# Kernel optimization log

Measured on AMD Instinct MI355X. Metric: run time of the kernel, lower is better.

## Reference

```python
import jax, jax.numpy as jnp
import numpy as np

P = 7                 # ROI pool output size (7,7)
SCALE = 1.0 / 16.0    # spatial_scale


def setup_inputs() -> dict:
    key = jax.random.key(0)
    ks = jax.random.split(key, 8)
    C, H, W = 512, 32, 32
    N = 128
    n_classes = 21
    features = jax.random.normal(ks[0], (1, C, H, W), dtype=jnp.float32)
    img_h, img_w = H * 16, W * 16  # image-space size implied by stride 16
    u = jax.random.uniform(ks[1], (N, 4), dtype=jnp.float32)
    x1 = u[:, 0] * (img_w - 32.0)
    y1 = u[:, 1] * (img_h - 32.0)
    x2 = x1 + 16.0 + u[:, 2] * (img_w - 1.0 - 16.0 - x1)
    y2 = y1 + 16.0 + u[:, 3] * (img_h - 1.0 - 16.0 - y1)
    rois = jnp.stack([jnp.zeros(N), x1, y1, x2, y2], axis=1).astype(jnp.float32)
    d_in = C * P * P

    def lin(k, fi, fo):
        return (jax.random.normal(k, (fi, fo), dtype=jnp.float32) / np.float32(np.sqrt(fi)))

    return {
        "features": features,
        "rois": rois,
        "W6": lin(ks[2], d_in, 4096), "b6": jnp.zeros((4096,), jnp.float32),
        "W7": lin(ks[3], 4096, 4096), "b7": jnp.zeros((4096,), jnp.float32),
        "Ws": lin(ks[4], 4096, n_classes), "bs": jnp.zeros((n_classes,), jnp.float32),
        "Wb": lin(ks[5], 4096, n_classes * 4), "bb": jnp.zeros((n_classes * 4,), jnp.float32),
    }


def roi_adaptive_max_pool(features, rois):
    # features: [1, C, H, W]; rois: [N, 5] (col 0 = batch idx, stripped as in torch)
    feats = features[0]                       # [C, H, W]
    C, H, W = feats.shape
    boxes = jnp.floor(rois[:, 1:] * SCALE).astype(jnp.int32)  # .long() trunc, coords >= 0
    x1, y1, x2, y2 = boxes[:, 0], boxes[:, 1], boxes[:, 2], boxes[:, 3]
    h = y2 - y1 + 1  # inclusive slicing roi[1]:roi[3]+1
    w = x2 - x1 + 1
    i = jnp.arange(P)
    # AdaptiveMaxPool2d bin boundaries: start = floor(i*h/P), end = ceil((i+1)*h/P)
    rs = y1[:, None] + (i[None, :] * h[:, None]) // P                       # [N, P]
    re = y1[:, None] + ((i[None, :] + 1) * h[:, None] + (P - 1)) // P
    cs = x1[:, None] + (i[None, :] * w[:, None]) // P
    ce = x1[:, None] + ((i[None, :] + 1) * w[:, None] + (P - 1)) // P
    MBr = -(-H // P)  # max rows per bin
    MBc = -(-W // P)  # max cols per bin
    neg_inf = jnp.float32(-jnp.inf)
    # row stage: max over each bin's rows, all columns kept
    ridx = rs[:, :, None] + jnp.arange(MBr)                                 # [N, P, MBr]
    rmask = ridx < re[:, :, None]
    ridx = jnp.clip(ridx, 0, H - 1)
    rowg = feats[:, ridx, :]                                                # [C, N, P, MBr, W]
    rowg = jnp.where(rmask[None, :, :, :, None], rowg, neg_inf)
    rowmax = rowg.max(axis=3).transpose(1, 0, 2, 3)                         # [N, C, P, W]
    # col stage: max over each bin's columns
    cidx = cs[:, :, None] + jnp.arange(MBc)                                 # [N, P, MBc]
    cmask = cidx < ce[:, :, None]
    cidx = jnp.clip(cidx, 0, W - 1)
    colg = jax.vmap(lambda rm, ci: rm[:, :, ci])(rowmax, cidx)              # [N, C, P, P, MBc]
    colg = jnp.where(cmask[:, None, None, :, :], colg, neg_inf)
    return colg.max(axis=-1)                                                # [N, C, P, P]


def reference(features, rois, W6, b6, W7, b7, Ws, bs, Wb, bb):
    pooled = roi_adaptive_max_pool(features, rois)          # [N, C, 7, 7]
    x = pooled.reshape(pooled.shape[0], -1)                 # [N, C*49]
    x = jax.nn.relu(x @ W6 + b6)                            # fc6 (dropout off: eval)
    x = jax.nn.relu(x @ W7 + b7)                            # fc7
    cls_prob = jax.nn.softmax(x @ Ws + bs, axis=1)          # [N, n_classes]
    bbox_pred = x @ Wb + bb                                 # [N, n_classes*4]
    return jnp.concatenate([cls_prob, bbox_pred], axis=1)   # [N, n_classes*5]
```

## Files before the change

kernel.cpp:

```cpp
#include <hip/hip_runtime.h>
#include <stdint.h>
#include <math.h>


typedef short short8 __attribute__((ext_vector_type(8)));
typedef float f32x4 __attribute__((ext_vector_type(4)));

__device__ __forceinline__ uint32_t pack_hilo(float x) {
  uint32_t xb = __float_as_uint(x);
  uint32_t hi = (xb + 0x7fffu + ((xb >> 16) & 1u)) >> 16;
  float hf = __uint_as_float(hi << 16);
  float d = x - hf;
  uint32_t db = __float_as_uint(d);
  uint32_t lo = (db + 0x7fffu + ((db >> 16) & 1u)) >> 16;
  return (lo << 16) | (hi & 0xffffu);
}

__device__ __forceinline__ void pack_pair(float x0, float x1,
                                          uint32_t& hw, uint32_t& lw) {
  uint32_t u0 = __float_as_uint(x0), u1 = __float_as_uint(x1);
  uint32_t r0 = (u0 + 0x7fffu + ((u0 >> 16) & 1u)) & 0xffff0000u;
  uint32_t r1 = (u1 + 0x7fffu + ((u1 >> 16) & 1u)) & 0xffff0000u;
  hw = r1 | (r0 >> 16);
  float d0 = x0 - __uint_as_float(r0);
  float d1 = x1 - __uint_as_float(r1);
  uint32_t v0 = __float_as_uint(d0), v1 = __float_as_uint(d1);
  uint32_t s0 = (v0 + 0x7fffu + ((v0 >> 16) & 1u)) & 0xffff0000u;
  uint32_t s1 = (v1 + 0x7fffu + ((v1 >> 16) & 1u)) & 0xffff0000u;
  lw = s1 | (s0 >> 16);
}

__device__ __forceinline__ short8 lds_frag(const uint32_t* p) {
  union { uint4 q; short8 s; } x;
  x.q = *(const uint4*)p;
  return x.s;
}

__global__ void transpose_k(const float* __restrict__ in, float* __restrict__ out) {
  __shared__ float sm[64][65];
  int bc = blockIdx.x & 7;
  int bp = blockIdx.x >> 3;
  int c0 = bc * 64, p0 = bp * 64;
  int tx = threadIdx.x & 63, ty = threadIdx.x >> 6;
  for (int r = ty; r < 64; r += 4)
    sm[r][tx] = in[(size_t)(c0 + r) * 1024 + p0 + tx];
  __syncthreads();
  for (int r = ty; r < 64; r += 4)
    out[(size_t)(p0 + r) * 512 + c0 + tx] = sm[tx][r];
}

__global__ void pool_k(const float* __restrict__ feats_t, const float* __restrict__ rois,
                       uint32_t* __restrict__ Ahi, uint32_t* __restrict__ Alo) {
  int n = blockIdx.x >> 1, half = blockIdx.x & 1;
  int t = threadIdx.x;
  int c = half * 256 + t;
  __shared__ uint32_t sm[256 * 49];

  float r1 = rois[n * 5 + 1], r2 = rois[n * 5 + 2];
  float r3 = rois[n * 5 + 3], r4 = rois[n * 5 + 4];
  int x1 = (int)floorf(r1 * 0.0625f);
  int y1 = (int)floorf(r2 * 0.0625f);
  int x2 = (int)floorf(r3 * 0.0625f);
  int y2 = (int)floorf(r4 * 0.0625f);
  int h = y2 - y1 + 1, w = x2 - x1 + 1;

  for (int cell = 0; cell < 49; ++cell) {
    int i = cell / 7, j = cell % 7;
    int rs = y1 + (i * h) / 7;
    int re = y1 + ((i + 1) * h + 6) / 7;  re = min(re, rs + 5);
    int cs = x1 + (j * w) / 7;
    int ce = x1 + ((j + 1) * w + 6) / 7;  ce = min(ce, cs + 5);
    float m = -INFINITY;
    for (int r = rs; r < re; ++r)
      for (int cc = cs; cc < ce; ++cc)
        m = fmaxf(m, feats_t[(size_t)(r * 32 + cc) * 512 + c]);
    sm[t * 49 + cell] = pack_hilo(m);
  }
  __syncthreads();
  uint32_t* dh = Ahi + (size_t)n * 12544 + (size_t)half * 6272;
  uint32_t* dl = Alo + (size_t)n * 12544 + (size_t)half * 6272;
  for (int i = t; i < 6272; i += 256) {
    uint32_t w0 = sm[2 * i], w1 = sm[2 * i + 1];
    dh[i] = __builtin_amdgcn_perm(w1, w0, 0x05040100u);
    dl[i] = __builtin_amdgcn_perm(w1, w0, 0x07060302u);
  }
}

__global__ __launch_bounds__(256, 2)
void gemm_splitk(const uint32_t* __restrict__ Ahi, const uint32_t* __restrict__ Alo,
                 const float* __restrict__ W, float* __restrict__ partials,
                 int Khalf, int ksteps, int ksh) {
  const int t = threadIdx.x;
  const int wvid = t >> 6, lane = t & 63;
  const int nb = blockIdx.x >> ksh;
  const int ks = blockIdx.x & ((1 << ksh) - 1);
  const int n0 = nb << 7;
  const int kbase2 = ks * (ksteps << 4);

  __shared__ uint32_t lds[4][128 * 20];

  const int nloc = t & 127, khalf = t >> 7;
  const float* wg = W + ((size_t)kbase2 * 2 + khalf * 16) * 4096 + n0 + nloc;

  const int arow = wvid * 32 + (lane >> 1);
  const int aco = (lane & 1) * 8;
  const uint32_t* agh = Ahi + (size_t)arow * Khalf + kbase2 + aco;
  const uint32_t* agl = Alo + (size_t)arow * Khalf + kbase2 + aco;

  f32x4 acc[2][8];
#pragma unroll
  for (int i = 0; i < 2; i++)
#pragma unroll
    for (int j = 0; j < 8; j++) acc[i][j] = f32x4{0.f, 0.f, 0.f, 0.f};

  float wcA[16], wcB[16];
  uint4 aA[4], aB[4];

  auto issue = [&](float (&wc)[16], uint4 (&av)[4], int s) {
    const float* wp = wg + (size_t)s * 32 * 4096;
#pragma unroll
    for (int i = 0; i < 16; i++) wc[i] = __builtin_nontemporal_load(wp + (size_t)i * 4096);
    const uint32_t* ph = agh + (size_t)s * 16;
    const uint32_t* pl = agl + (size_t)s * 16;
    av[0] = *(const uint4*)(ph);
    av[1] = *(const uint4*)(ph + 4);
    av[2] = *(const uint4*)(pl);
    av[3] = *(const uint4*)(pl + 4);
  };

  auto pack_w = [&](float (&wc)[16], uint32_t (&hw)[8], uint32_t (&lw)[8]) {
#pragma unroll
    for (int j = 0; j < 8; j++) pack_pair(wc[2 * j], wc[2 * j + 1], hw[j], lw[j]);
  };
  auto store_tile = [&](uint32_t (&hw)[8], uint32_t (&lw)[8], uint4 (&av)[4]) {
    *(uint4*)&lds[2][nloc * 20 + khalf * 8]     = make_uint4(hw[0], hw[1], hw[2], hw[3]);
    *(uint4*)&lds[2][nloc * 20 + khalf * 8 + 4] = make_uint4(hw[4], hw[5], hw[6], hw[7]);
    *(uint4*)&lds[3][nloc * 20 + khalf * 8]     = make_uint4(lw[0], lw[1], lw[2], lw[3]);
    *(uint4*)&lds[3][nloc * 20 + khalf * 8 + 4] = make_uint4(lw[4], lw[5], lw[6], lw[7]);
    *(uint4*)&lds[0][arow * 20 + aco]     = av[0];
    *(uint4*)&lds[0][arow * 20 + aco + 4] = av[1];
    *(uint4*)&lds[1][arow * 20 + aco]     = av[2];
    *(uint4*)&lds[1][arow * 20 + aco + 4] = av[3];
  };

  const int lr = lane & 15, kk = lane >> 4;

  auto mfma_tile = [&]() {
    short8 ahif[2], alof[2];
#pragma unroll
    for (int fm = 0; fm < 2; fm++) {
      int rb = (wvid * 32 + fm * 16 + lr) * 20 + kk * 4;
      ahif[fm] = lds_frag(&lds[0][rb]);
      alof[fm] = lds_frag(&lds[1][rb]);
    }
#pragma unroll
    for (int fn = 0; fn < 8; fn++) {
      int rb = (fn * 16 + lr) * 20 + kk * 4;
      short8 bhi = lds_frag(&lds[2][rb]);
      short8 blo = lds_frag(&lds[3][rb]);
#pragma unroll
      for (int fm = 0; fm < 2; fm++) {
        acc[fm][fn] = __builtin_amdgcn_mfma_f32_16x16x32_bf16(ahif[fm], bhi, acc[fm][fn], 0, 0, 0);
        acc[fm][fn] = __builtin_amdgcn_mfma_f32_16x16x32_bf16(ahif[fm], blo, acc[fm][fn], 0, 0, 0);
        acc[fm][fn] = __builtin_amdgcn_mfma_f32_16x16x32_bf16(alof[fm], bhi, acc[fm][fn], 0, 0, 0);
      }
    }
  };

  issue(wcA, aA, 0);
  if (ksteps > 1) issue(wcB, aB, 1);
  {
    uint32_t hw[8], lw[8];
    pack_w(wcA, hw, lw);
    store_tile(hw, lw, aA);
  }
  __syncthreads();

  for (int s = 0; s < ksteps; s += 2) {
    if (s + 2 < ksteps) issue(wcA, aA, s + 2);
    mfma_tile();
    if (s + 1 < ksteps) {
      uint32_t hw[8], lw[8];
      pack_w(wcB, hw, lw);
      __syncthreads();
      store_tile(hw, lw, aB);
      __syncthreads();
      if (s + 3 < ksteps) issue(wcB, aB, s + 3);
      mfma_tile();
      if (s + 2 < ksteps) {
        uint32_t hw2[8], lw2[8];
        pack_w(wcA, hw2, lw2);
        __syncthreads();
        store_tile(hw2, lw2, aA);
        __syncthreads();
      }
    }
  }

  float* pout = partials + (size_t)ks * 524288;
  const int rq = lane >> 4;
#pragma unroll
  for (int fm = 0; fm < 2; fm++)
#pragma unroll
    for (int fn = 0; fn < 8; fn++)
#pragma unroll
      for (int r = 0; r < 4; r++) {
        int row = wvid * 32 + fm * 16 + rq * 4 + r;
        int col = n0 + fn * 16 + lr;
        __builtin_nontemporal_store(acc[fm][fn][r], pout + (size_t)row * 4096 + col);
      }
}

__global__ void reduce_k(const float* __restrict__ partials, const float* __restrict__ bias,
                         uint32_t* __restrict__ outhi, uint32_t* __restrict__ outlo,
                         float* __restrict__ fout, int KS) {
  int idx = blockIdx.x * 256 + threadIdx.x;
  int base = idx * 4;
  float4 s = make_float4(0.f, 0.f, 0.f, 0.f);
  for (int k = 0; k < KS; k++) {
    const float4 p = *(const float4*)(partials + (size_t)k * 524288 + base);
    s.x += p.x; s.y += p.y; s.z += p.z; s.w += p.w;
  }
  const float4 bv = *(const float4*)(bias + (base & 4095));
  s.x = fmaxf(s.x + bv.x, 0.f); s.y = fmaxf(s.y + bv.y, 0.f);
  s.z = fmaxf(s.z + bv.z, 0.f); s.w = fmaxf(s.w + bv.w, 0.f);
  if (outhi) {
    uint32_t h0, l0, h1, l1;
    pack_pair(s.x, s.y, h0, l0);
    pack_pair(s.z, s.w, h1, l1);
    *(uint2*)(outhi + idx * 2) = make_uint2(h0, h1);
    *(uint2*)(outlo + idx * 2) = make_uint2(l0, l1);
  } else {
    *(float4*)(fout + base) = s;
  }
}

__global__ void heads_k(const float* __restrict__ x2, const float* __restrict__ Ws,
                        const float* __restrict__ bs, const float* __restrict__ Wb,
                        const float* __restrict__ bb, float* __restrict__ out) {
  int n = blockIdx.x, t = threadIdx.x;
  int j = t & 127, kq = t >> 7;
  float a0 = 0.f, a1 = 0.f, a2 = 0.f, a3 = 0.f;
  if (j < 105) {
    const float* xp = x2 + (size_t)n * 4096 + kq * 1024;
    const float* wq;
    int stride;
    if (j < 21) { wq = Ws + (size_t)kq * 1024 * 21 + j; stride = 21; }
    else        { wq = Wb + (size_t)kq * 1024 * 84 + (j - 21); stride = 84; }
    for (int k = 0; k < 1024; k += 4) {
      const float4 xv = *(const float4*)(xp + k);
      a0 += xv.x * wq[(size_t)k * stride];
      a1 += xv.y * wq[(size_t)(k + 1) * stride];
      a2 += xv.z * wq[(size_t)(k + 2) * stride];
      a3 += xv.w * wq[(size_t)(k + 3) * stride];
    }
  }
  __shared__ float sacc[512];
  __shared__ float slog[105];
  sacc[t] = (a0 + a1) + (a2 + a3);
  __syncthreads();
  if (t < 105)
    slog[t] = (sacc[t] + sacc[t + 128]) + (sacc[t + 256] + sacc[t + 384]) +
              (t < 21 ? bs[t] : bb[t - 21]);
  __syncthreads();
  if (t < 105) {
    float v = slog[t];
    if (t < 21) {
      float m = slog[0];
      for (int q = 1; q < 21; q++) m = fmaxf(m, slog[q]);
      float ssum = 0.f;
      for (int q = 0; q < 21; q++) ssum += expf(slog[q] - m);
      v = expf(v - m) / ssum;
    }
    out[(size_t)n * 105 + t] = v;
  }
}

extern "C" void kernel_launch(void* const* d_in, const int* in_sizes, int n_in,
                              void* d_out, int out_size, void* d_ws, size_t ws_size,
                              hipStream_t stream) {
  const float* feats = (const float*)d_in[0];
  const float* rois  = (const float*)d_in[1];
  const float* W6 = (const float*)d_in[2];
  const float* b6 = (const float*)d_in[3];
  const float* W7 = (const float*)d_in[4];
  const float* b7 = (const float*)d_in[5];
  const float* Wsp = (const float*)d_in[6];
  const float* bsp = (const float*)d_in[7];
  const float* Wbp = (const float*)d_in[8];
  const float* bbp = (const float*)d_in[9];
  float* out = (float*)d_out;

  char* ws = (char*)d_ws;
  size_t o = 0;
  float*    feats_t = (float*)(ws + o);    o += (size_t)512 * 1024 * 4;
  uint32_t* Ahi     = (uint32_t*)(ws + o); o += (size_t)128 * 12544 * 4;
  uint32_t* Alo     = (uint32_t*)(ws + o); o += (size_t)128 * 12544 * 4;
  uint32_t* A2hi    = (uint32_t*)(ws + o); o += (size_t)128 * 2048 * 4;
  uint32_t* A2lo    = (uint32_t*)(ws + o); o += (size_t)128 * 2048 * 4;
  float*    x2      = (float*)(ws + o);    o += (size_t)128 * 4096 * 4;
  size_t fixed = o;
  int KS = 16;
  while (KS > 1 && fixed + (size_t)KS * 524288 * 4 > ws_size) KS >>= 1;
  float* partials = (float*)(ws + o);
  int ksh = (KS == 16) ? 4 : (KS == 8) ? 3 : (KS == 4) ? 2 : (KS == 2) ? 1 : 0;
  int ksh7 = (ksh > 3) ? 3 : ksh;
  int KS7 = 1 << ksh7;

  hipLaunchKernelGGL(transpose_k, dim3(128), dim3(256), 0, stream, feats, feats_t);
  hipLaunchKernelGGL(pool_k, dim3(256), dim3(256), 0, stream, feats_t, rois, Ahi, Alo);
  hipLaunchKernelGGL(gemm_splitk, dim3(32 << ksh), dim3(256), 0, stream,
                     Ahi, Alo, W6, partials, 12544, 25088 / (KS * 32), ksh);
  hipLaunchKernelGGL(reduce_k, dim3(512), dim3(256), 0, stream,
                     partials, b6, A2hi, A2lo, (float*)nullptr, KS);
  hipLaunchKernelGGL(gemm_splitk, dim3(32 << ksh7), dim3(256), 0, stream,
                     A2hi, A2lo, W7, partials, 2048, 4096 / (KS7 * 32), ksh7);
  hipLaunchKernelGGL(reduce_k, dim3(512), dim3(256), 0, stream,
                     partials, b7, (uint32_t*)nullptr, (uint32_t*)nullptr, x2, KS7);
  hipLaunchKernelGGL(heads_k, dim3(128), dim3(512), 0, stream,
                     x2, Wsp, bsp, Wbp, bbp, out);
}
```

Baseline: 932.0 us.

## Drop LDS staging in split-K GEMM; load MFMA fragments straight from registers/global

The GEMM kernel no longer stages A and W tiles through shared memory with barriers. Each wave now loads its W fragment directly into registers in MFMA B-operand order and packs it in place. A is read directly from global memory in a new fragment-friendly transposed layout (k-quad major, row, 4 words), which pool_k and reduce_k now write. fc7 also uses the full split-K factor instead of capping it at 8. The aim is to remove LDS traffic and __syncthreads stalls. The cost is redundant global/L2 reads of A across waves, more registers, and scattered writes in pool and reduce.

Result: faster. 899.7 us (-3.5%).

```diff
diff --git a/kernel.cpp b/kernel.cpp
--- a/kernel.cpp
+++ b/kernel.cpp
@@ -30,9 +30,14 @@
   lw = s1 | (s0 >> 16);
 }
 
-__device__ __forceinline__ short8 lds_frag(const uint32_t* p) {
+__device__ __forceinline__ short8 u4_to_s8(uint4 q) {
   union { uint4 q; short8 s; } x;
-  x.q = *(const uint4*)p;
+  x.q = q;
+  return x.s;
+}
+__device__ __forceinline__ short8 mk8(uint32_t a, uint32_t b, uint32_t c, uint32_t d) {
+  union { uint32_t u[4]; short8 s; } x;
+  x.u[0] = a; x.u[1] = b; x.u[2] = c; x.u[3] = d;
   return x.s;
 }
 
@@ -50,7 +55,7 @@
 }
 
 __global__ void pool_k(const float* __restrict__ feats_t, const float* __restrict__ rois,
-                       uint32_t* __restrict__ Ahi, uint32_t* __restrict__ Alo) {
+                       uint32_t* __restrict__ AhiT, uint32_t* __restrict__ AloT) {
   int n = blockIdx.x >> 1, half = blockIdx.x & 1;
   int t = threadIdx.x;
   int c = half * 256 + t;
@@ -77,135 +82,95 @@
     sm[t * 49 + cell] = pack_hilo(m);
   }
   __syncthreads();
-  uint32_t* dh = Ahi + (size_t)n * 12544 + (size_t)half * 6272;
-  uint32_t* dl = Alo + (size_t)n * 12544 + (size_t)half * 6272;
   for (int i = t; i < 6272; i += 256) {
     uint32_t w0 = sm[2 * i], w1 = sm[2 * i + 1];
-    dh[i] = __builtin_amdgcn_perm(w1, w0, 0x05040100u);
-    dl[i] = __builtin_amdgcn_perm(w1, w0, 0x07060302u);
+    int kp = half * 6272 + i;
+    size_t ad = ((size_t)(kp >> 2) * 128 + n) * 4 + (kp & 3);
+    AhiT[ad] = __builtin_amdgcn_perm(w1, w0, 0x05040100u);
+    AloT[ad] = __builtin_amdgcn_perm(w1, w0, 0x07060302u);
   }
 }
 
 __global__ __launch_bounds__(256, 2)
-void gemm_splitk(const uint32_t* __restrict__ Ahi, const uint32_t* __restrict__ Alo,
-                 const float* __restrict__ W, float* __restrict__ partials,
-                 int Khalf, int ksteps, int ksh) {
-  const int t = threadIdx.x;
-  const int wvid = t >> 6, lane = t & 63;
-  const int nb = blockIdx.x >> ksh;
-  const int ks = blockIdx.x & ((1 << ksh) - 1);
-  const int n0 = nb << 7;
-  const int kbase2 = ks * (ksteps << 4);
-
-  __shared__ uint32_t lds[4][128 * 20];
-
-  const int nloc = t & 127, khalf = t >> 7;
-  const float* wg = W + ((size_t)kbase2 * 2 + khalf * 16) * 4096 + n0 + nloc;
-
-  const int arow = wvid * 32 + (lane >> 1);
-  const int aco = (lane & 1) * 8;
-  const uint32_t* agh = Ahi + (size_t)arow * Khalf + kbase2 + aco;
-  const uint32_t* agl = Alo + (size_t)arow * Khalf + kbase2 + aco;
-
-  f32x4 acc[2][8];
-#pragma unroll
-  for (int i = 0; i < 2; i++)
-#pragma unroll
-    for (int j = 0; j < 8; j++) acc[i][j] = f32x4{0.f, 0.f, 0.f, 0.f};
-
-  float wcA[16], wcB[16];
-  uint4 aA[4], aB[4];
-
-  auto issue = [&](float (&wc)[16], uint4 (&av)[4], int s) {
-    const float* wp = wg + (size_t)s * 32 * 4096;
-#pragma unroll
-    for (int i = 0; i < 16; i++) wc[i] = __builtin_nontemporal_load(wp + (size_t)i * 4096);
-    const uint32_t* ph = agh + (size_t)s * 16;
-    const uint32_t* pl = agl + (size_t)s * 16;
-    av[0] = *(const uint4*)(ph);
-    av[1] = *(const uint4*)(ph + 4);
-    av[2] = *(const uint4*)(pl);
-    av[3] = *(const uint4*)(pl + 4);
+void gemm_nb(const uint32_t* __restrict__ AhiT, const uint32_t* __restrict__ AloT,
+             const float* __restrict__ W, float* __restrict__ partials,
+             int ksteps, int ksh) {
+  const int t = threadIdx.x, wv = t >> 6, lane = t & 63;
+  const int lr = lane & 15, kk = lane >> 4;
+  const int nb = blockIdx.x >> ksh, ks = blockIdx.x & ((1 << ksh) - 1);
+  const int n0 = (nb << 7) + wv * 32;
+  const int kp40 = ks * ksteps * 4;
+
+  const float* wg = W + ((size_t)kp40 * 8 + kk * 8) * 4096 + n0 + lr;
+  const uint32_t* ah = AhiT + ((size_t)(kp40 + kk) * 128 + lr) * 4;
+  const uint32_t* al = AloT + ((size_t)(kp40 + kk) * 128 + lr) * 4;
+
+  f32x4 acc[8][2];
+#pragma unroll
+  for (int i = 0; i < 8; i++)
+#pragma unroll
+    for (int j = 0; j < 2; j++) acc[i][j] = f32x4{0.f, 0.f, 0.f, 0.f};
+
+  float wA[16], wB[16];
+
+  auto wissue = [&](float (&wc)[16], int s) {
+    const float* p = wg + (size_t)s * 32 * 4096;
+#pragma unroll
+    for (int fn = 0; fn < 2; fn++)
+#pragma unroll
+      for (int j = 0; j < 8; j++)
+        wc[fn * 8 + j] = __builtin_nontemporal_load(p + (size_t)j * 4096 + fn * 16);
   };
 
-  auto pack_w = [&](float (&wc)[16], uint32_t (&hw)[8], uint32_t (&lw)[8]) {
-#pragma unroll
-    for (int j = 0; j < 8; j++) pack_pair(wc[2 * j], wc[2 * j + 1], hw[j], lw[j]);
+  auto do_tile = [&](int s, float (&wc)[16]) {
+    uint4 ahv[8], alv[8];
+    const uint32_t* pa = ah + (size_t)s * 2048;
+    const uint32_t* pl = al + (size_t)s * 2048;
+#pragma unroll
+    for (int fm = 0; fm < 8; fm++) {
+      ahv[fm] = *(const uint4*)(pa + fm * 64);
+      alv[fm] = *(const uint4*)(pl + fm * 64);
+    }
+    uint32_t bh[2][4], bl[2][4];
+#pragma unroll
+    for (int fn = 0; fn < 2; fn++)
+#pragma unroll
+      for (int jj = 0; jj < 4; jj++)
+        pack_pair(wc[fn * 8 + 2 * jj], wc[fn * 8 + 2 * jj + 1], bh[fn][jj], bl[fn][jj]);
+#pragma unroll
+    for (int fn = 0; fn < 2; fn++) {
+      short8 b_hi = mk8(bh[fn][0], bh[fn][1], bh[fn][2], bh[fn][3]);
+      short8 b_lo = mk8(bl[fn][0], bl[fn][1], bl[fn][2], bl[fn][3]);
+#pragma unroll
+      for (int fm = 0; fm < 8; fm++) {
+        short8 a_hi = u4_to_s8(ahv[fm]);
+        short8 a_lo = u4_to_s8(alv[fm]);
+        acc[fm][fn] = __builtin_amdgcn_mfma_f32_16x16x32_bf16(a_hi, b_hi, acc[fm][fn], 0, 0, 0);
+        acc[fm][fn] = __builtin_amdgcn_mfma_f32_16x16x32_bf16(a_hi, b_lo, acc[fm][fn], 0, 0, 0);
+        acc[fm][fn] = __builtin_amdgcn_mfma_f32_16x16x32_bf16(a_lo, b_hi, acc[fm][fn], 0, 0, 0);
+      }
+    }
   };
-  auto store_tile = [&](uint32_t (&hw)[8], uint32_t (&lw)[8], uint4 (&av)[4]) {
-    *(uint4*)&lds[2][nloc * 20 + khalf * 8]     = make_uint4(hw[0], hw[1], hw[2], hw[3]);
-    *(uint4*)&lds[2][nloc * 20 + khalf * 8 + 4] = make_uint4(hw[4], hw[5], hw[6], hw[7]);
-    *(uint4*)&lds[3][nloc * 20 + khalf * 8]     = make_uint4(lw[0], lw[1], lw[2], lw[3]);
-    *(uint4*)&lds[3][nloc * 20 + khalf * 8 + 4] = make_uint4(lw[4], lw[5], lw[6], lw[7]);
-    *(uint4*)&lds[0][arow * 20 + aco]     = av[0];
-    *(uint4*)&lds[0][arow * 20 + aco + 4] = av[1];
-    *(uint4*)&lds[1][arow * 20 + aco]     = av[2];
-    *(uint4*)&lds[1][arow * 20 + aco + 4] = av[3];
-  };
-
-  const int lr = lane & 15, kk = lane >> 4;
-
-  auto mfma_tile = [&]() {
-    short8 ahif[2], alof[2];
-#pragma unroll
-    for (int fm = 0; fm < 2; fm++) {
-      int rb = (wvid * 32 + fm * 16 + lr) * 20 + kk * 4;
-      ahif[fm] = lds_frag(&lds[0][rb]);
-      alof[fm] = lds_frag(&lds[1][rb]);
-    }
-#pragma unroll
-    for (int fn = 0; fn < 8; fn++) {
-      int rb = (fn * 16 + lr) * 20 + kk * 4;
-      short8 bhi = lds_frag(&lds[2][rb]);
-      short8 blo = lds_frag(&lds[3][rb]);
-#pragma unroll
-      for (int fm = 0; fm < 2; fm++) {
-        acc[fm][fn] = __builtin_amdgcn_mfma_f32_16x16x32_bf16(ahif[fm], bhi, acc[fm][fn], 0, 0, 0);
-        acc[fm][fn] = __builtin_amdgcn_mfma_f32_16x16x32_bf16(ahif[fm], blo, acc[fm][fn], 0, 0, 0);
-        acc[fm][fn] = __builtin_amdgcn_mfma_f32_16x16x32_bf16(alof[fm], bhi, acc[fm][fn], 0, 0, 0);
-      }
-    }
-  };
-
-  issue(wcA, aA, 0);
-  if (ksteps > 1) issue(wcB, aB, 1);
-  {
-    uint32_t hw[8], lw[8];
-    pack_w(wcA, hw, lw);
-    store_tile(hw, lw, aA);
-  }
-  __syncthreads();
-
+
+  wissue(wA, 0);
   for (int s = 0; s < ksteps; s += 2) {
-    if (s + 2 < ksteps) issue(wcA, aA, s + 2);
-    mfma_tile();
+    if (s + 1 < ksteps) wissue(wB, s + 1);
+    do_tile(s, wA);
     if (s + 1 < ksteps) {
-      uint32_t hw[8], lw[8];
-      pack_w(wcB, hw, lw);
-      __syncthreads();
-      store_tile(hw, lw, aB);
-      __syncthreads();
-      if (s + 3 < ksteps) issue(wcB, aB, s + 3);
-      mfma_tile();
-      if (s + 2 < ksteps) {
-        uint32_t hw2[8], lw2[8];
-        pack_w(wcA, hw2, lw2);
-        __syncthreads();
-        store_tile(hw2, lw2, aA);
-        __syncthreads();
-      }
+      if (s + 2 < ksteps) wissue(wA, s + 2);
+      do_tile(s + 1, wB);
     }
   }
 
   float* pout = partials + (size_t)ks * 524288;
   const int rq = lane >> 4;
 #pragma unroll
-  for (int fm = 0; fm < 2; fm++)
-#pragma unroll
-    for (int fn = 0; fn < 8; fn++)
+  for (int fm = 0; fm < 8; fm++)
+#pragma unroll
+    for (int fn = 0; fn < 2; fn++)
 #pragma unroll
       for (int r = 0; r < 4; r++) {
-        int row = wvid * 32 + fm * 16 + rq * 4 + r;
+        int row = fm * 16 + rq * 4 + r;
         int col = n0 + fn * 16 + lr;
         __builtin_nontemporal_store(acc[fm][fn][r], pout + (size_t)row * 4096 + col);
       }
@@ -228,8 +193,10 @@
     uint32_t h0, l0, h1, l1;
     pack_pair(s.x, s.y, h0, l0);
     pack_pair(s.z, s.w, h1, l1);
-    *(uint2*)(outhi + idx * 2) = make_uint2(h0, h1);
-    *(uint2*)(outlo + idx * 2) = make_uint2(l0, l1);
+    int r = base >> 12, c = base & 4095, kp0 = c >> 1;
+    size_t ad = ((size_t)(kp0 >> 2) * 128 + r) * 4 + (kp0 & 3);
+    *(uint2*)(outhi + ad) = make_uint2(h0, h1);
+    *(uint2*)(outlo + ad) = make_uint2(l0, l1);
   } else {
     *(float4*)(fout + base) = s;
   }
@@ -294,8 +261,8 @@
   char* ws = (char*)d_ws;
   size_t o = 0;
   float*    feats_t = (float*)(ws + o);    o += (size_t)512 * 1024 * 4;
-  uint32_t* Ahi     = (uint32_t*)(ws + o); o += (size_t)128 * 12544 * 4;
-  uint32_t* Alo     = (uint32_t*)(ws + o); o += (size_t)128 * 12544 * 4;
+  uint32_t* AhiT    = (uint32_t*)(ws + o); o += (size_t)128 * 12544 * 4;
+  uint32_t* AloT    = (uint32_t*)(ws + o); o += (size_t)128 * 12544 * 4;
   uint32_t* A2hi    = (uint32_t*)(ws + o); o += (size_t)128 * 2048 * 4;
   uint32_t* A2lo    = (uint32_t*)(ws + o); o += (size_t)128 * 2048 * 4;
   float*    x2      = (float*)(ws + o);    o += (size_t)128 * 4096 * 4;
@@ -304,19 +271,17 @@
   while (KS > 1 && fixed + (size_t)KS * 524288 * 4 > ws_size) KS >>= 1;
   float* partials = (float*)(ws + o);
   int ksh = (KS == 16) ? 4 : (KS == 8) ? 3 : (KS == 4) ? 2 : (KS == 2) ? 1 : 0;
-  int ksh7 = (ksh > 3) ? 3 : ksh;
-  int KS7 = 1 << ksh7;
 
   hipLaunchKernelGGL(transpose_k, dim3(128), dim3(256), 0, stream, feats, feats_t);
-  hipLaunchKernelGGL(pool_k, dim3(256), dim3(256), 0, stream, feats_t, rois, Ahi, Alo);
-  hipLaunchKernelGGL(gemm_splitk, dim3(32 << ksh), dim3(256), 0, stream,
-                     Ahi, Alo, W6, partials, 12544, 25088 / (KS * 32), ksh);
+  hipLaunchKernelGGL(pool_k, dim3(256), dim3(256), 0, stream, feats_t, rois, AhiT, AloT);
+  hipLaunchKernelGGL(gemm_nb, dim3(32 << ksh), dim3(256), 0, stream,
+                     AhiT, AloT, W6, partials, 25088 / (KS * 32), ksh);
   hipLaunchKernelGGL(reduce_k, dim3(512), dim3(256), 0, stream,
                      partials, b6, A2hi, A2lo, (float*)nullptr, KS);
-  hipLaunchKernelGGL(gemm_splitk, dim3(32 << ksh7), dim3(256), 0, stream,
-                     A2hi, A2lo, W7, partials, 2048, 4096 / (KS7 * 32), ksh7);
+  hipLaunchKernelGGL(gemm_nb, dim3(32 << ksh), dim3(256), 0, stream,
+                     A2hi, A2lo, W7, partials, 4096 / (KS * 32), ksh);
   hipLaunchKernelGGL(reduce_k, dim3(512), dim3(256), 0, stream,
-                     partials, b7, (uint32_t*)nullptr, (uint32_t*)nullptr, x2, KS7);
+                     partials, b7, (uint32_t*)nullptr, (uint32_t*)nullptr, x2, KS);
   hipLaunchKernelGGL(heads_k, dim3(128), dim3(512), 0, stream,
                      x2, Wsp, bsp, Wbp, bbp, out);
 }
```
